# Optimization experiments

Hardware: AMD Instinct MI355X
Metric: run time of the kernel (lower is better)

Reference implementation:

```python
import jax, jax.numpy as jnp
import numpy as np

B = 1048576
H = 256


def _parity_W():
    # W[i,j,k] = 1 if (i+j+k+1) % 2 == 0  <=>  (i+j+k) odd
    idx = jnp.arange(2)
    s = idx[:, None, None] + idx[None, :, None] + idx[None, None, :]
    return (s % 2 == 1).astype(jnp.float32)


def setup_inputs() -> dict:
    key = jax.random.key(0)
    ks = jax.random.split(key, 7)
    x = jax.random.normal(ks[0], (B, 3), dtype=jnp.float32)
    w1 = jax.random.normal(ks[1], (H, 3), dtype=jnp.float32) * (1.0 / np.sqrt(3))
    b1 = jax.random.normal(ks[2], (H,), dtype=jnp.float32) * 0.01
    w2 = jax.random.normal(ks[3], (H, H), dtype=jnp.float32) * (1.0 / np.sqrt(H))
    b2 = jax.random.normal(ks[4], (H,), dtype=jnp.float32) * 0.01
    w3 = jax.random.normal(ks[5], (3, H), dtype=jnp.float32) * (1.0 / np.sqrt(H))
    b3 = jax.random.normal(ks[6], (3,), dtype=jnp.float32) * 0.01
    return {"x": x, "w1": w1, "b1": b1, "w2": w2, "b2": b2, "w3": w3, "b3": b3}


def reference(x, w1, b1, w2, b2, w3, b3):
    # MLP: 3 -> H -> H -> 3 with ReLU
    h = jax.nn.relu(x @ w1.T + b1)          # (B, H)
    h = jax.nn.relu(h @ w2.T + b2)          # (B, H)
    logitC = h @ w3.T + b3                  # (B, 3)

    eps = 1e-05
    sig = jax.nn.sigmoid(logitC)            # (B, 3)
    p_pos = (sig + eps) / (1.0 + 2.0 * eps)
    p_neg = (1.0 - sig + eps) / (1.0 + 2.0 * eps)
    p = jnp.stack([p_neg, p_pos], axis=-1)  # (B, 3, 2): per-concept Bernoulli probs

    W = _parity_W()                          # (2, 2, 2) XOR-parity indicator
    pred1 = jnp.einsum('bi,bj,bk,ijk->b', p[:, 0], p[:, 1], p[:, 2], W)  # (B,)
    pred = jnp.stack([1.0 - pred1, pred1], axis=1)  # (B, 2)
    pred = (pred + 0.001) / (1.0 + 2.0 * 0.001)
    return pred, logitC
```

## Files before the change

kernel.cpp:

```cpp
#include <hip/hip_runtime.h>

typedef _Float16 f16;
typedef _Float16 f16x8 __attribute__((ext_vector_type(8)));
typedef float f32x16 __attribute__((ext_vector_type(16)));
typedef unsigned int u32;
typedef unsigned int u32x4 __attribute__((ext_vector_type(4)));

#define THREADS 512
#define MTILE   128
#define NBLK    256

#define H1_OFF   0
#define XS_OFF   131072
#define PART_OFF 134144
#define LDS_BYTES 158720

template <int I0>
static __device__ __forceinline__ u32x4 relu_pack8(const f32x16& h) {
  const float c0 = fmaxf(h[I0+0], 0.f), c1 = fmaxf(h[I0+1], 0.f);
  const float c2 = fmaxf(h[I0+2], 0.f), c3 = fmaxf(h[I0+3], 0.f);
  const float c4 = fmaxf(h[I0+4], 0.f), c5 = fmaxf(h[I0+5], 0.f);
  const float c6 = fmaxf(h[I0+6], 0.f), c7 = fmaxf(h[I0+7], 0.f);
  u32 P = __builtin_bit_cast(u32, __builtin_amdgcn_cvt_pkrtz(c0, c1));
  u32 Q = __builtin_bit_cast(u32, __builtin_amdgcn_cvt_pkrtz(c2, c3));
  u32 R = __builtin_bit_cast(u32, __builtin_amdgcn_cvt_pkrtz(c4, c5));
  u32 S = __builtin_bit_cast(u32, __builtin_amdgcn_cvt_pkrtz(c6, c7));
  asm("v_permlane32_swap_b32 %0, %1" : "+v"(P), "+v"(R));
  asm("v_permlane32_swap_b32 %0, %1" : "+v"(Q), "+v"(S));
  u32x4 w; w[0] = P; w[1] = Q; w[2] = R; w[3] = S;
  return w;
}

__global__ __launch_bounds__(THREADS, 1)
void fused_mlp_parity(const float* __restrict__ x,
                      const float* __restrict__ w1,
                      const float* __restrict__ b1,
                      const float* __restrict__ w2,
                      const float* __restrict__ b2,
                      const float* __restrict__ w3,
                      const float* __restrict__ b3,
                      float* __restrict__ out, int Bsz) {
  __shared__ __align__(128) unsigned char lds[LDS_BYTES];
  const int tid  = threadIdx.x;
  const int lane = tid & 63;
  const int wave = tid >> 6;
  const int arow = lane & 31;
  const int half = lane >> 5;

  const int ntiles = Bsz / MTILE;
  const int tpb    = ntiles / NBLK;
  const int t0     = blockIdx.x * tpb;

  float* xsf   = (float*)(lds + XS_OFF);
  float* partf = (float*)(lds + PART_OFF);

  {
    const float4* xg = (const float4*)x;
    float4* xv = (float4*)xsf;
    if (tid < 96)                      xv[tid]        = xg[(size_t)t0*96 + tid];
    else if (tid >= 128 && tid < 224)  xv[96 + tid-128] = xg[(size_t)(t0+1)*96 + (tid-128)];
  }

  const int col = (wave << 5) + arow;
  f16x8 w2A[16];
#pragma unroll
  for (int ks = 0; ks < 16; ++ks) {
    const float* src = w2 + (size_t)col*256 + ks*16 + half*8;
    float4 u0 = *(const float4*)src;
    float4 u1 = *(const float4*)(src + 4);
    f16x8 v;
    v[0]=(f16)u0.x; v[1]=(f16)u0.y; v[2]=(f16)u0.z; v[3]=(f16)u0.w;
    v[4]=(f16)u1.x; v[5]=(f16)u1.y; v[6]=(f16)u1.z; v[7]=(f16)u1.w;
    w2A[ks] = v;
  }
  f16x8 w1A = {};
  if (half == 0) {
    w1A[0] = (f16)w1[col*3+0]; w1A[1] = (f16)w1[col*3+1];
    w1A[2] = (f16)w1[col*3+2]; w1A[3] = (f16)b1[col];
  }
  f16x8 b2A = {};  if (half == 0) b2A[0] = (f16)b2[col];
  f16x8 ones = {}; if (half == 0) ones[0] = (f16)1.0f;
  f16x8 w3A[2];
#pragma unroll
  for (int q = 0; q < 2; ++q) {
    f16x8 v = {};
    if (arow < 3) {
#pragma unroll
      for (int j = 0; j < 8; ++j)
        v[j] = (f16)w3[arow*256 + (wave<<5) + q*16 + half*8 + j];
    }
    w3A[q] = v;
  }
  const float b3r0 = b3[0], b3r1 = b3[1], b3r2 = b3[2];
  const size_t outL = (size_t)Bsz * 2;
  const u32 rk = ((u32)(arow & 15)) << 4;

  auto PHASE_B = [&](int buf) {
    unsigned char* h1b = lds + H1_OFF + (u32)buf*65536;
    const float* xb_src = xsf + (u32)buf*384;
#pragma unroll
    for (int nt = 0; nt < 4; ++nt) {
      const int r = nt*32 + arow;
      f16x8 xb = {};
      if (half == 0) {
        const float* xr = xb_src + r*3;
        xb[0] = (f16)xr[0]; xb[1] = (f16)xr[1]; xb[2] = (f16)xr[2];
        xb[3] = (f16)1.0f;
      }
      f32x16 h = {};
      h = __builtin_amdgcn_mfma_f32_32x32x16_f16(w1A, xb, h, 0,0,0);
      const u32 rowbase = ((u32)r << 9);
      {
        u32x4 w = relu_pack8<0>(h);
        const u32 slot = (u32)(((wave<<5) + 0*16)*2 + half*16);
        *(u32x4*)(h1b + rowbase + (slot ^ rk)) = w;
      }
      {
        u32x4 w = relu_pack8<8>(h);
        const u32 slot = (u32)(((wave<<5) + 1*16)*2 + half*16);
        *(u32x4*)(h1b + rowbase + (slot ^ rk)) = w;
      }
    }
  };

  __syncthreads();
  PHASE_B(0);
  __syncthreads();

  for (int tl = 0; tl < tpb; ++tl) {
    const int cur = tl & 1, nxt = cur ^ 1;
    const unsigned char* h1b = lds + H1_OFF + (u32)cur*65536;
    const u32 cb = (u32)half << 4;

#pragma unroll
    for (int ntp = 0; ntp < 2; ++ntp) {
      f32x16 acc0, acc1;
      {
        f32x16 z = {};
        acc0 = __builtin_amdgcn_mfma_f32_32x32x16_f16(b2A, ones, z, 0,0,0);
        acc1 = __builtin_amdgcn_mfma_f32_32x32x16_f16(b2A, ones, z, 0,0,0);
      }
      const u32 row0 = (u32)((ntp*2 + 0)*32 + arow) << 9;
      const u32 row1 = (u32)((ntp*2 + 1)*32 + arow) << 9;
#pragma unroll
      for (int ks = 0; ks < 16; ++ks) {
        const u32 coff = ((((u32)ks) << 5) + cb) ^ rk;
        f16x8 fr0 = *(const f16x8*)(h1b + row0 + coff);
        f16x8 fr1 = *(const f16x8*)(h1b + row1 + coff);
        acc0 = __builtin_amdgcn_mfma_f32_32x32x16_f16(w2A[ks], fr0, acc0, 0,0,0);
        acc1 = __builtin_amdgcn_mfma_f32_32x32x16_f16(w2A[ks], fr1, acc1, 0,0,0);
      }
#pragma unroll
      for (int p = 0; p < 2; ++p) {
        const f32x16& a = p ? acc1 : acc0;
        const int nt = ntp*2 + p;
        f32x16 a3 = {};
        {
          u32x4 w = relu_pack8<0>(a);
          a3 = __builtin_amdgcn_mfma_f32_32x32x16_f16(w3A[0], __builtin_bit_cast(f16x8, w), a3, 0,0,0);
        }
        {
          u32x4 w = relu_pack8<8>(a);
          a3 = __builtin_amdgcn_mfma_f32_32x32x16_f16(w3A[1], __builtin_bit_cast(f16x8, w), a3, 0,0,0);
        }
        if (half == 0) {
          float* pr = partf + (u32)cur*3072 + (u32)((wave<<7) + nt*32 + arow)*3;
          pr[0] = a3[0]; pr[1] = a3[1]; pr[2] = a3[2];
        }
      }
    }

    if (tl + 1 < tpb) PHASE_B(nxt);

    if (tl + 2 < tpb && tid >= 416) {
      const int i = tid - 416;
      ((float4*)(xsf + (u32)cur*384))[i] =
          ((const float4*)x)[(size_t)(t0 + tl + 2)*96 + i];
    }

    if (tl > 0 && tid < MTILE) {
      const int r = tid;
      const float* pb = partf + (u32)nxt*3072;
      float l0 = b3r0, l1 = b3r1, l2 = b3r2;
#pragma unroll
      for (int w8 = 0; w8 < 8; ++w8) {
        const float* pr = pb + (u32)((w8<<7) + r)*3;
        l0 += pr[0]; l1 += pr[1]; l2 += pr[2];
      }
      const float inv1p2e = 1.0f / (1.0f + 2.0f * 1e-5f);
      const float tt0 = (1.0f - 2.0f / (1.0f + __expf(-l0))) * inv1p2e;
      const float tt1 = (1.0f - 2.0f / (1.0f + __expf(-l1))) * inv1p2e;
      const float tt2 = (1.0f - 2.0f / (1.0f + __expf(-l2))) * inv1p2e;
      const float pred1 = 0.5f * (1.0f - tt0 * tt1 * tt2);
      const size_t grow = (size_t)(t0 + tl - 1)*MTILE + r;
      float2 ov;
      ov.x = (1.0f - pred1 + 0.001f) * (1.0f / 1.002f);
      ov.y = (pred1 + 0.001f) * (1.0f / 1.002f);
      *(float2*)(out + grow*2) = ov;
      out[outL + grow*3 + 0] = l0;
      out[outL + grow*3 + 1] = l1;
      out[outL + grow*3 + 2] = l2;
    }
    __syncthreads();
  }

  if (tid < MTILE) {
    const int r = tid;
    const float* pb = partf + (u32)((tpb - 1) & 1)*3072;
    float l0 = b3r0, l1 = b3r1, l2 = b3r2;
#pragma unroll
    for (int w8 = 0; w8 < 8; ++w8) {
      const float* pr = pb + (u32)((w8<<7) + r)*3;
      l0 += pr[0]; l1 += pr[1]; l2 += pr[2];
    }
    const float inv1p2e = 1.0f / (1.0f + 2.0f * 1e-5f);
    const float tt0 = (1.0f - 2.0f / (1.0f + __expf(-l0))) * inv1p2e;
    const float tt1 = (1.0f - 2.0f / (1.0f + __expf(-l1))) * inv1p2e;
    const float tt2 = (1.0f - 2.0f / (1.0f + __expf(-l2))) * inv1p2e;
    const float pred1 = 0.5f * (1.0f - tt0 * tt1 * tt2);
    const size_t grow = (size_t)(t0 + tpb - 1)*MTILE + r;
    float2 ov;
    ov.x = (1.0f - pred1 + 0.001f) * (1.0f / 1.002f);
    ov.y = (pred1 + 0.001f) * (1.0f / 1.002f);
    *(float2*)(out + grow*2) = ov;
    out[outL + grow*3 + 0] = l0;
    out[outL + grow*3 + 1] = l1;
    out[outL + grow*3 + 2] = l2;
  }
}

extern "C" void kernel_launch(void* const* d_in, const int* in_sizes, int n_in,
                              void* d_out, int out_size, void* d_ws, size_t ws_size,
                              hipStream_t stream) {
  const float* x  = (const float*)d_in[0];
  const float* w1 = (const float*)d_in[1];
  const float* b1 = (const float*)d_in[2];
  const float* w2 = (const float*)d_in[3];
  const float* b2 = (const float*)d_in[4];
  const float* w3 = (const float*)d_in[5];
  const float* b3 = (const float*)d_in[6];
  float* out = (float*)d_out;
  const int Bsz = in_sizes[0] / 3;

  dim3 grid(NBLK), block(THREADS);
  fused_mlp_parity<<<grid, block, 0, stream>>>(x, w1, b1, w2, b2, w3, b3, out, Bsz);
}
```

Baseline: 218.1 us.

## Drop LDS double-buffering to fit two blocks per CU and double grid

After: 260.3 us. +19.3%, slower.

```diff
diff --git a/kernel.cpp b/kernel.cpp
--- a/kernel.cpp
+++ b/kernel.cpp
@@ -8,12 +8,12 @@
 
 #define THREADS 512
 #define MTILE   128
-#define NBLK    256
+#define NBLK    512
 
 #define H1_OFF   0
-#define XS_OFF   131072
-#define PART_OFF 134144
-#define LDS_BYTES 158720
+#define XS_OFF   65536
+#define PART_OFF 68608
+#define LDS_BYTES 80896
 
 template <int I0>
 static __device__ __forceinline__ u32x4 relu_pack8(const f32x16& h) {
@@ -31,7 +31,7 @@
   return w;
 }
 
-__global__ __launch_bounds__(THREADS, 1)
+__global__ __launch_bounds__(THREADS, 4)
 void fused_mlp_parity(const float* __restrict__ x,
                       const float* __restrict__ w1,
                       const float* __restrict__ b1,
@@ -54,12 +54,7 @@
   float* xsf   = (float*)(lds + XS_OFF);
   float* partf = (float*)(lds + PART_OFF);
 
-  {
-    const float4* xg = (const float4*)x;
-    float4* xv = (float4*)xsf;
-    if (tid < 96)                      xv[tid]        = xg[(size_t)t0*96 + tid];
-    else if (tid >= 128 && tid < 224)  xv[96 + tid-128] = xg[(size_t)(t0+1)*96 + (tid-128)];
-  }
+  if (tid < 96) ((float4*)xsf)[tid] = ((const float4*)x)[(size_t)t0*96 + tid];
 
   const int col = (wave << 5) + arow;
   f16x8 w2A[16];
@@ -94,43 +89,45 @@
   const float b3r0 = b3[0], b3r1 = b3[1], b3r2 = b3[2];
   const size_t outL = (size_t)Bsz * 2;
   const u32 rk = ((u32)(arow & 15)) << 4;
-
-  auto PHASE_B = [&](int buf) {
-    unsigned char* h1b = lds + H1_OFF + (u32)buf*65536;
-    const float* xb_src = xsf + (u32)buf*384;
-#pragma unroll
-    for (int nt = 0; nt < 4; ++nt) {
-      const int r = nt*32 + arow;
-      f16x8 xb = {};
-      if (half == 0) {
-        const float* xr = xb_src + r*3;
-        xb[0] = (f16)xr[0]; xb[1] = (f16)xr[1]; xb[2] = (f16)xr[2];
-        xb[3] = (f16)1.0f;
-      }
-      f32x16 h = {};
-      h = __builtin_amdgcn_mfma_f32_32x32x16_f16(w1A, xb, h, 0,0,0);
-      const u32 rowbase = ((u32)r << 9);
-      {
-        u32x4 w = relu_pack8<0>(h);
-        const u32 slot = (u32)(((wave<<5) + 0*16)*2 + half*16);
-        *(u32x4*)(h1b + rowbase + (slot ^ rk)) = w;
-      }
-      {
-        u32x4 w = relu_pack8<8>(h);
-        const u32 slot = (u32)(((wave<<5) + 1*16)*2 + half*16);
-        *(u32x4*)(h1b + rowbase + (slot ^ rk)) = w;
-      }
-    }
-  };
-
-  __syncthreads();
-  PHASE_B(0);
+  const u32 cb = (u32)half << 4;
+
   __syncthreads();
 
   for (int tl = 0; tl < tpb; ++tl) {
     const int cur = tl & 1, nxt = cur ^ 1;
-    const unsigned char* h1b = lds + H1_OFF + (u32)cur*65536;
-    const u32 cb = (u32)half << 4;
+
+    {
+      const float* xb_src = xsf + (u32)cur*384;
+#pragma unroll
+      for (int nt = 0; nt < 4; ++nt) {
+        const int r = nt*32 + arow;
+        f16x8 xb = {};
+        if (half == 0) {
+          const float* xr = xb_src + r*3;
+          xb[0] = (f16)xr[0]; xb[1] = (f16)xr[1]; xb[2] = (f16)xr[2];
+          xb[3] = (f16)1.0f;
+        }
+        f32x16 h = {};
+        h = __builtin_amdgcn_mfma_f32_32x32x16_f16(w1A, xb, h, 0,0,0);
+        const u32 rowbase = ((u32)r << 9);
+        {
+          u32x4 w = relu_pack8<0>(h);
+          const u32 slot = (u32)(((wave<<5) + 0)*2 + half*16);
+          *(u32x4*)(lds + H1_OFF + rowbase + (slot ^ rk)) = w;
+        }
+        {
+          u32x4 w = relu_pack8<8>(h);
+          const u32 slot = (u32)(((wave<<5) + 16)*2 + half*16);
+          *(u32x4*)(lds + H1_OFF + rowbase + (slot ^ rk)) = w;
+        }
+      }
+    }
+    if (tl + 1 < tpb && tid >= 416) {
+      const int i = tid - 416;
+      ((float4*)(xsf + (u32)nxt*384))[i] =
+          ((const float4*)x)[(size_t)(t0 + tl + 1)*96 + i];
+    }
+    __syncthreads();
 
 #pragma unroll
     for (int ntp = 0; ntp < 2; ++ntp) {
@@ -145,8 +142,8 @@
 #pragma unroll
       for (int ks = 0; ks < 16; ++ks) {
         const u32 coff = ((((u32)ks) << 5) + cb) ^ rk;
-        f16x8 fr0 = *(const f16x8*)(h1b + row0 + coff);
-        f16x8 fr1 = *(const f16x8*)(h1b + row1 + coff);
+        f16x8 fr0 = *(const f16x8*)(lds + H1_OFF + row0 + coff);
+        f16x8 fr1 = *(const f16x8*)(lds + H1_OFF + row1 + coff);
         acc0 = __builtin_amdgcn_mfma_f32_32x32x16_f16(w2A[ks], fr0, acc0, 0,0,0);
         acc1 = __builtin_amdgcn_mfma_f32_32x32x16_f16(w2A[ks], fr1, acc1, 0,0,0);
       }
@@ -164,27 +161,19 @@
           a3 = __builtin_amdgcn_mfma_f32_32x32x16_f16(w3A[1], __builtin_bit_cast(f16x8, w), a3, 0,0,0);
         }
         if (half == 0) {
-          float* pr = partf + (u32)cur*3072 + (u32)((wave<<7) + nt*32 + arow)*3;
+          float* pr = partf + (u32)((wave<<7) + nt*32 + arow)*3;
           pr[0] = a3[0]; pr[1] = a3[1]; pr[2] = a3[2];
         }
       }
     }
-
-    if (tl + 1 < tpb) PHASE_B(nxt);
-
-    if (tl + 2 < tpb && tid >= 416) {
-      const int i = tid - 416;
-      ((float4*)(xsf + (u32)cur*384))[i] =
-          ((const float4*)x)[(size_t)(t0 + tl + 2)*96 + i];
-    }
-
-    if (tl > 0 && tid < MTILE) {
+    __syncthreads();
+
+    if (tid < MTILE) {
       const int r = tid;
-      const float* pb = partf + (u32)nxt*3072;
       float l0 = b3r0, l1 = b3r1, l2 = b3r2;
 #pragma unroll
       for (int w8 = 0; w8 < 8; ++w8) {
-        const float* pr = pb + (u32)((w8<<7) + r)*3;
+        const float* pr = partf + (u32)((w8<<7) + r)*3;
         l0 += pr[0]; l1 += pr[1]; l2 += pr[2];
       }
       const float inv1p2e = 1.0f / (1.0f + 2.0f * 1e-5f);
@@ -192,7 +181,7 @@
       const float tt1 = (1.0f - 2.0f / (1.0f + __expf(-l1))) * inv1p2e;
       const float tt2 = (1.0f - 2.0f / (1.0f + __expf(-l2))) * inv1p2e;
       const float pred1 = 0.5f * (1.0f - tt0 * tt1 * tt2);
-      const size_t grow = (size_t)(t0 + tl - 1)*MTILE + r;
+      const size_t grow = (size_t)(t0 + tl)*MTILE + r;
       float2 ov;
       ov.x = (1.0f - pred1 + 0.001f) * (1.0f / 1.002f);
       ov.y = (pred1 + 0.001f) * (1.0f / 1.002f);
@@ -201,31 +190,6 @@
       out[outL + grow*3 + 1] = l1;
       out[outL + grow*3 + 2] = l2;
     }
-    __syncthreads();
-  }
-
-  if (tid < MTILE) {
-    const int r = tid;
-    const float* pb = partf + (u32)((tpb - 1) & 1)*3072;
-    float l0 = b3r0, l1 = b3r1, l2 = b3r2;
-#pragma unroll
-    for (int w8 = 0; w8 < 8; ++w8) {
-      const float* pr = pb + (u32)((w8<<7) + r)*3;
-      l0 += pr[0]; l1 += pr[1]; l2 += pr[2];
-    }
-    const float inv1p2e = 1.0f / (1.0f + 2.0f * 1e-5f);
-    const float tt0 = (1.0f - 2.0f / (1.0f + __expf(-l0))) * inv1p2e;
-    const float tt1 = (1.0f - 2.0f / (1.0f + __expf(-l1))) * inv1p2e;
-    const float tt2 = (1.0f - 2.0f / (1.0f + __expf(-l2))) * inv1p2e;
-    const float pred1 = 0.5f * (1.0f - tt0 * tt1 * tt2);
-    const size_t grow = (size_t)(t0 + tpb - 1)*MTILE + r;
-    float2 ov;
-    ov.x = (1.0f - pred1 + 0.001f) * (1.0f / 1.002f);
-    ov.y = (pred1 + 0.001f) * (1.0f / 1.002f);
-    *(float2*)(out + grow*2) = ov;
-    out[outL + grow*3 + 0] = l0;
-    out[outL + grow*3 + 1] = l1;
-    out[outL + grow*3 + 2] = l2;
   }
 }
 
```

## Stagger phase order between wave groups to overlap MFMA and LDS work

Applied to the files above, without the earlier changes.

After: 218.9 us. About the same (+0.3%).

```diff
diff --git a/kernel.cpp b/kernel.cpp
--- a/kernel.cpp
+++ b/kernel.cpp
@@ -46,6 +46,7 @@
   const int wave = tid >> 6;
   const int arow = lane & 31;
   const int half = lane >> 5;
+  const int grp  = wave >> 2;
 
   const int ntiles = Bsz / MTILE;
   const int tpb    = ntiles / NBLK;
@@ -56,9 +57,8 @@
 
   {
     const float4* xg = (const float4*)x;
-    float4* xv = (float4*)xsf;
-    if (tid < 96)                      xv[tid]        = xg[(size_t)t0*96 + tid];
-    else if (tid >= 128 && tid < 224)  xv[96 + tid-128] = xg[(size_t)(t0+1)*96 + (tid-128)];
+    if (tid < 96)                      ((float4*)xsf)[tid]            = xg[(size_t)t0*96 + tid];
+    else if (tid >= 128 && tid < 224)  ((float4*)xsf)[96 + tid - 128] = xg[(size_t)(t0+1)*96 + (tid-128)];
   }
 
   const int col = (wave << 5) + arow;
@@ -94,6 +94,7 @@
   const float b3r0 = b3[0], b3r1 = b3[1], b3r2 = b3[2];
   const size_t outL = (size_t)Bsz * 2;
   const u32 rk = ((u32)(arow & 15)) << 4;
+  const u32 cb = (u32)half << 4;
 
   auto PHASE_B = [&](int buf) {
     unsigned char* h1b = lds + H1_OFF + (u32)buf*65536;
@@ -112,26 +113,19 @@
       const u32 rowbase = ((u32)r << 9);
       {
         u32x4 w = relu_pack8<0>(h);
-        const u32 slot = (u32)(((wave<<5) + 0*16)*2 + half*16);
+        const u32 slot = (u32)(((wave<<5) + 0)*2 + half*16);
         *(u32x4*)(h1b + rowbase + (slot ^ rk)) = w;
       }
       {
         u32x4 w = relu_pack8<8>(h);
-        const u32 slot = (u32)(((wave<<5) + 1*16)*2 + half*16);
+        const u32 slot = (u32)(((wave<<5) + 16)*2 + half*16);
         *(u32x4*)(h1b + rowbase + (slot ^ rk)) = w;
       }
     }
   };
 
-  __syncthreads();
-  PHASE_B(0);
-  __syncthreads();
-
-  for (int tl = 0; tl < tpb; ++tl) {
-    const int cur = tl & 1, nxt = cur ^ 1;
-    const unsigned char* h1b = lds + H1_OFF + (u32)cur*65536;
-    const u32 cb = (u32)half << 4;
-
+  auto PHASE_CE = [&](int buf) {
+    const unsigned char* h1b = lds + H1_OFF + (u32)buf*65536;
 #pragma unroll
     for (int ntp = 0; ntp < 2; ++ntp) {
       f32x16 acc0, acc1;
@@ -164,23 +158,18 @@
           a3 = __builtin_amdgcn_mfma_f32_32x32x16_f16(w3A[1], __builtin_bit_cast(f16x8, w), a3, 0,0,0);
         }
         if (half == 0) {
-          float* pr = partf + (u32)cur*3072 + (u32)((wave<<7) + nt*32 + arow)*3;
+          float* pr = partf + (u32)buf*3072 + (u32)((wave<<7) + nt*32 + arow)*3;
           pr[0] = a3[0]; pr[1] = a3[1]; pr[2] = a3[2];
         }
       }
     }
-
-    if (tl + 1 < tpb) PHASE_B(nxt);
-
-    if (tl + 2 < tpb && tid >= 416) {
-      const int i = tid - 416;
-      ((float4*)(xsf + (u32)cur*384))[i] =
-          ((const float4*)x)[(size_t)(t0 + tl + 2)*96 + i];
-    }
-
-    if (tl > 0 && tid < MTILE) {
-      const int r = tid;
-      const float* pb = partf + (u32)nxt*3072;
+  };
+
+  auto FINAL = [&](int pbuf, int tidx) {
+    const int idx = tid - 256;
+    if (idx >= 0 && idx < MTILE) {
+      const int r = idx;
+      const float* pb = partf + (u32)pbuf*3072;
       float l0 = b3r0, l1 = b3r1, l2 = b3r2;
 #pragma unroll
       for (int w8 = 0; w8 < 8; ++w8) {
@@ -192,7 +181,7 @@
       const float tt1 = (1.0f - 2.0f / (1.0f + __expf(-l1))) * inv1p2e;
       const float tt2 = (1.0f - 2.0f / (1.0f + __expf(-l2))) * inv1p2e;
       const float pred1 = 0.5f * (1.0f - tt0 * tt1 * tt2);
-      const size_t grow = (size_t)(t0 + tl - 1)*MTILE + r;
+      const size_t grow = (size_t)(t0 + tidx)*MTILE + r;
       float2 ov;
       ov.x = (1.0f - pred1 + 0.001f) * (1.0f / 1.002f);
       ov.y = (pred1 + 0.001f) * (1.0f / 1.002f);
@@ -201,32 +190,32 @@
       out[outL + grow*3 + 1] = l1;
       out[outL + grow*3 + 2] = l2;
     }
+  };
+
+  __syncthreads();
+  PHASE_B(0);
+  __syncthreads();
+
+  for (int tl = 0; tl < tpb; ++tl) {
+    const int cur = tl & 1, nxt = cur ^ 1;
+
+    if (grp == 0) {
+      PHASE_CE(cur);
+      if (tl + 1 < tpb) PHASE_B(nxt);
+      if (tl + 2 < tpb && tid >= 128 && tid < 224) {
+        const int i = tid - 128;
+        ((float4*)(xsf + (u32)cur*384))[i] =
+            ((const float4*)x)[(size_t)(t0 + tl + 2)*96 + i];
+      }
+    } else {
+      if (tl + 1 < tpb) PHASE_B(nxt);
+      PHASE_CE(cur);
+      if (tl > 0) FINAL(nxt, tl - 1);
+    }
     __syncthreads();
   }
 
-  if (tid < MTILE) {
-    const int r = tid;
-    const float* pb = partf + (u32)((tpb - 1) & 1)*3072;
-    float l0 = b3r0, l1 = b3r1, l2 = b3r2;
-#pragma unroll
-    for (int w8 = 0; w8 < 8; ++w8) {
-      const float* pr = pb + (u32)((w8<<7) + r)*3;
-      l0 += pr[0]; l1 += pr[1]; l2 += pr[2];
-    }
-    const float inv1p2e = 1.0f / (1.0f + 2.0f * 1e-5f);
-    const float tt0 = (1.0f - 2.0f / (1.0f + __expf(-l0))) * inv1p2e;
-    const float tt1 = (1.0f - 2.0f / (1.0f + __expf(-l1))) * inv1p2e;
-    const float tt2 = (1.0f - 2.0f / (1.0f + __expf(-l2))) * inv1p2e;
-    const float pred1 = 0.5f * (1.0f - tt0 * tt1 * tt2);
-    const size_t grow = (size_t)(t0 + tpb - 1)*MTILE + r;
-    float2 ov;
-    ov.x = (1.0f - pred1 + 0.001f) * (1.0f / 1.002f);
-    ov.y = (pred1 + 0.001f) * (1.0f / 1.002f);
-    *(float2*)(out + grow*2) = ov;
-    out[outL + grow*3 + 0] = l0;
-    out[outL + grow*3 + 1] = l1;
-    out[outL + grow*3 + 2] = l2;
-  }
+  FINAL((tpb - 1) & 1, tpb - 1);
 }
 
 extern "C" void kernel_launch(void* const* d_in, const int* in_sizes, int n_in,
```
